# Optimization experiments

Measured on AMD Instinct MI355X. Metric: run time of the kernel, lower is better.

The kernel has to match this reference:

```python
import jax, jax.numpy as jnp
import numpy as np

B, N, F = 2, 100000, 64
E = 800000
E_OUT, N_OUT = 16, 64


def setup_inputs() -> dict:
    key = jax.random.key(0)
    ks = jax.random.split(key, 8)
    x = jax.random.normal(ks[0], (B, N, F), dtype=jnp.float32)
    edge_src = jax.random.randint(ks[1], (E,), 0, N, dtype=jnp.int32)
    edge_target = jax.random.randint(ks[2], (E,), 0, N, dtype=jnp.int32)
    edge_weight = jax.random.uniform(ks[3], (E, 1), dtype=jnp.float32)
    in_dim = 2 * F + 1  # 129
    W_e = jax.random.normal(ks[4], (in_dim, E_OUT), dtype=jnp.float32) / np.sqrt(in_dim)
    b_e = jnp.zeros((E_OUT,), dtype=jnp.float32)
    W_n = jax.random.normal(ks[5], (E_OUT, N_OUT), dtype=jnp.float32) / np.sqrt(E_OUT)
    b_n = jnp.zeros((N_OUT,), dtype=jnp.float32)
    return {"x": x, "edge_src": edge_src, "edge_target": edge_target,
            "edge_weight": edge_weight, "W_e": W_e, "b_e": b_e,
            "W_n": W_n, "b_n": b_n}


def reference(x, edge_src, edge_target, edge_weight, W_e, b_e, W_n, b_n):
    # gather endpoint features: [B, E, F]
    node_src = x[:, edge_src]
    node_target = x[:, edge_target]
    # per-edge learned scalar weight broadcast over batch: [B, E, 1]
    ew = jnp.broadcast_to(edge_weight[None, :, :], (x.shape[0], edge_weight.shape[0], 1))
    h = jnp.concatenate([node_src, node_target, ew], axis=-1)  # [B, E, 2F+1]
    h = jax.nn.sigmoid(h @ W_e + b_e)                           # edge MLP -> [B, E, 16]
    # scatter_add(+h at target) + scatter_add(-h at src) -> [B, N, 16]
    agg = jnp.zeros((x.shape[0], x.shape[1], h.shape[-1]), dtype=h.dtype)
    agg = agg.at[:, edge_target].add(h).at[:, edge_src].add(-h)
    out = jax.nn.sigmoid(agg @ W_n + b_n)                       # node MLP -> [B, N, out_dim]
    return out
```

## Files before the change

### kernel.cpp

```cpp
#include <hip/hip_runtime.h>
#include <hip/hip_fp16.h>

#define NB 2
#define NN 100000
#define NF 64
#define NE 800000
#define EO 16
#define NO 64
#define QS 512.0f

__device__ __forceinline__ float sigmoidf(float v) {
    return 1.0f / (1.0f + __expf(-v));
}

__global__ __launch_bounds__(256) void pre_kernel(
    const float* __restrict__ x, const float* __restrict__ We,
    const float* __restrict__ be, __half* __restrict__ P1h,
    __half* __restrict__ P2h, float4* __restrict__ aggz)
{
    int u = blockIdx.x * 256 + threadIdx.x;
    if (u >= NB * NN) return;
    int b = u >= NN;
    int n = u - b * NN;

    if (!b) {
        float4 z = make_float4(0.f, 0.f, 0.f, 0.f);
#pragma unroll
        for (int q = 0; q < 4; ++q) aggz[(size_t)n * 4 + q] = z;
    }

    float a1[EO], a2[EO];
#pragma unroll
    for (int k = 0; k < EO; ++k) { a1[k] = 0.f; a2[k] = be[k]; }

    const float* row = x + (size_t)u * NF;
#pragma unroll 4
    for (int j4 = 0; j4 < 16; ++j4) {
        float4 v = *(const float4*)(row + 4 * j4);
        const float* w1 = We + (size_t)(4 * j4) * EO;
        const float* w2 = We + (size_t)(NF + 4 * j4) * EO;
#pragma unroll
        for (int jj = 0; jj < 4; ++jj) {
            float vv = ((const float*)&v)[jj];
#pragma unroll
            for (int k = 0; k < EO; ++k) {
                a1[k] += vv * w1[jj * EO + k];
                a2[k] += vv * w2[jj * EO + k];
            }
        }
    }

    __half2 h1[8], h2[8];
#pragma unroll
    for (int i = 0; i < 8; ++i) {
        h1[i] = __floats2half2_rn(a1[2 * i], a1[2 * i + 1]);
        h2[i] = __floats2half2_rn(a2[2 * i], a2[2 * i + 1]);
    }
    __half* p1 = P1h + (size_t)n * (NB * EO) + b * EO;
    __half* p2 = P2h + (size_t)n * (NB * EO) + b * EO;
    *(float4*)(p1)     = ((float4*)h1)[0];
    *(float4*)(p1 + 8) = ((float4*)h1)[1];
    *(float4*)(p2)     = ((float4*)h2)[0];
    *(float4*)(p2 + 8) = ((float4*)h2)[1];
}

__global__ __launch_bounds__(256) void edge_kernel(
    const int* __restrict__ esrc, const int* __restrict__ etgt,
    const float* __restrict__ ew, const __half* __restrict__ P1h,
    const __half* __restrict__ P2h, const float* __restrict__ We,
    unsigned long long* __restrict__ agg)
{
    __shared__ unsigned long long hbuf[256 * 9];
    __shared__ int snode[256];
    __shared__ int tnode[256];

    int tid = threadIdx.x;
    int e = blockIdx.x * 256 + tid;
    int s = esrc[e];
    int t = etgt[e];
    float w = ew[e];
    snode[tid] = s;
    tnode[tid] = t;

    const float* wr = We + (size_t)2 * NF * EO;

    float4 sv[4], tv[4];
    const float4* p1 = (const float4*)(P1h + (size_t)s * (NB * EO));
    const float4* p2 = (const float4*)(P2h + (size_t)t * (NB * EO));
#pragma unroll
    for (int i = 0; i < 4; ++i) { sv[i] = p1[i]; tv[i] = p2[i]; }

    const __half2* sh = (const __half2*)sv;
    const __half2* th = (const __half2*)tv;
    float hs[NB * EO];
#pragma unroll
    for (int i = 0; i < 16; ++i) {
        float2 fs = __half22float2(sh[i]);
        float2 ft = __half22float2(th[i]);
        hs[2 * i]     = sigmoidf(fs.x + ft.x + w * wr[(2 * i) & 15]);
        hs[2 * i + 1] = sigmoidf(fs.y + ft.y + w * wr[(2 * i + 1) & 15]);
    }

#pragma unroll
    for (int j = 0; j < 8; ++j) {
        long long q0 = __float2int_rn(hs[4 * j + 0] * QS);
        long long q1 = __float2int_rn(hs[4 * j + 1] * QS);
        long long q2 = __float2int_rn(hs[4 * j + 2] * QS);
        long long q3 = __float2int_rn(hs[4 * j + 3] * QS);
        hbuf[tid * 9 + j] =
            (unsigned long long)(q0 + (q1 << 16) + (q2 << 32) + (q3 << 48));
    }
    __syncthreads();

    int g = tid >> 3;
    int k8 = tid & 7;
#pragma unroll
    for (int i = 0; i < 8; ++i) {
        int el = g + (i << 5);
        unsigned long long v = hbuf[el * 9 + k8];
        int tt = tnode[el];
        int ss = snode[el];
        atomicAdd(agg + (size_t)tt * 8 + k8, v);
        atomicAdd(agg + (size_t)ss * 8 + k8, 0ULL - v);
    }
}

__global__ __launch_bounds__(256) void node_kernel(
    const unsigned long long* __restrict__ agg, const float* __restrict__ Wn,
    const float* __restrict__ bn, float* __restrict__ out)
{
    __shared__ float wn[EO * NO];
    int tid = threadIdx.x;
    {
        float4 wv = ((const float4*)Wn)[tid];
        wv.x *= (1.0f / QS); wv.y *= (1.0f / QS);
        wv.z *= (1.0f / QS); wv.w *= (1.0f / QS);
        *(float4*)(wn + tid * 4) = wv;
    }
    __syncthreads();

    int u = blockIdx.x * 256 + tid;
    int row = u >> 4;
    int q = u & 15;
    int b = row >= NN;
    int n = row - b * NN;

    const unsigned long long* ar = agg + ((size_t)n * NB + b) * 4;
    ulonglong2 w01 = ((const ulonglong2*)ar)[0];
    ulonglong2 w23 = ((const ulonglong2*)ar)[1];
    unsigned long long ww[4] = { w01.x, w01.y, w23.x, w23.y };

    float a[EO];
#pragma unroll
    for (int j = 0; j < 4; ++j) {
        unsigned long long wv = ww[j];
        int s0 = (short)(unsigned short)wv;
        wv = (wv - (unsigned long long)(long long)s0) >> 16;
        int s1 = (short)(unsigned short)wv;
        wv = (wv - (unsigned long long)(long long)s1) >> 16;
        int s2 = (short)(unsigned short)wv;
        wv = (wv - (unsigned long long)(long long)s2) >> 16;
        int s3 = (short)(unsigned short)wv;
        a[4 * j + 0] = (float)s0;
        a[4 * j + 1] = (float)s1;
        a[4 * j + 2] = (float)s2;
        a[4 * j + 3] = (float)s3;
    }

    float4 acc = *(const float4*)(bn + q * 4);
#pragma unroll
    for (int k = 0; k < EO; ++k) {
        float ak = a[k];
        float4 wv = *(const float4*)(wn + k * NO + q * 4);
        acc.x += ak * wv.x;
        acc.y += ak * wv.y;
        acc.z += ak * wv.z;
        acc.w += ak * wv.w;
    }
    float4 o = make_float4(sigmoidf(acc.x), sigmoidf(acc.y),
                           sigmoidf(acc.z), sigmoidf(acc.w));
    *(float4*)(out + (size_t)row * NO + q * 4) = o;
}

extern "C" void kernel_launch(void* const* d_in, const int* in_sizes, int n_in,
                              void* d_out, int out_size, void* d_ws, size_t ws_size,
                              hipStream_t stream) {
    const float* x    = (const float*)d_in[0];
    const int*   esrc = (const int*)d_in[1];
    const int*   etgt = (const int*)d_in[2];
    const float* ew   = (const float*)d_in[3];
    const float* We   = (const float*)d_in[4];
    const float* be   = (const float*)d_in[5];
    const float* Wn   = (const float*)d_in[6];
    const float* bn   = (const float*)d_in[7];
    float* out = (float*)d_out;

    unsigned long long* agg = (unsigned long long*)d_ws;
    __half* P1h = (__half*)((char*)d_ws + (size_t)NN * 8 * sizeof(unsigned long long));
    __half* P2h = P1h + (size_t)NN * NB * EO;

    pre_kernel<<<(NB * NN + 255) / 256, 256, 0, stream>>>(x, We, be, P1h, P2h,
                                                          (float4*)agg);
    edge_kernel<<<NE / 256, 256, 0, stream>>>(esrc, etgt, ew, P1h, P2h, We, agg);
    node_kernel<<<NB * NN * 16 / 256, 256, 0, stream>>>(agg, Wn, bn, out);
}
```

Measured before the change: 223.1 us.

## Stage node rows in shared memory for pre-kernel and split edge kernel into chunks

The pre-kernel now loads 64 node rows per block into padded shared memory. Each wave computes 8 of the 32 projection outputs (one half of W_e and one k-half), so per-thread register pressure drops and the global x reads are coalesced. Zeroing the aggregation buffer is spread over all threads. The edge kernel is launched as 8 sequential chunks via a block offset, perhaps to improve atomic locality or L2 residency, at the cost of extra launch overhead.

```diff
diff --git a/kernel.cpp b/kernel.cpp
--- a/kernel.cpp
+++ b/kernel.cpp
@@ -16,55 +16,58 @@
 __global__ __launch_bounds__(256) void pre_kernel(
     const float* __restrict__ x, const float* __restrict__ We,
     const float* __restrict__ be, __half* __restrict__ P1h,
-    __half* __restrict__ P2h, float4* __restrict__ aggz)
+    __half* __restrict__ P2h, unsigned long long* __restrict__ aggz)
 {
-    int u = blockIdx.x * 256 + threadIdx.x;
-    if (u >= NB * NN) return;
-    int b = u >= NN;
-    int n = u - b * NN;
-
-    if (!b) {
-        float4 z = make_float4(0.f, 0.f, 0.f, 0.f);
-#pragma unroll
-        for (int q = 0; q < 4; ++q) aggz[(size_t)n * 4 + q] = z;
-    }
-
-    float a1[EO], a2[EO];
-#pragma unroll
-    for (int k = 0; k < EO; ++k) { a1[k] = 0.f; a2[k] = be[k]; }
-
-    const float* row = x + (size_t)u * NF;
-#pragma unroll 4
+    __shared__ float xs[64 * 68];
+    int tid = threadIdx.x;
+    int bid = blockIdx.x;
+
+    aggz[(size_t)bid * 256 + tid] = 0ULL;
+
+    const float4* xsrc = (const float4*)(x + (size_t)bid * 64 * NF);
+#pragma unroll
+    for (int i = 0; i < 4; ++i) {
+        int f = i * 256 + tid;
+        int r = f >> 4, c4 = f & 15;
+        float4 v = xsrc[f];
+        *(float4*)&xs[r * 68 + c4 * 4] = v;
+    }
+    __syncthreads();
+
+    int r = tid & 63;
+    int wv = __builtin_amdgcn_readfirstlane(tid >> 6);
+    int half = wv & 1;
+    int kh = wv >> 1;
+    const float* wb = We + (size_t)half * NF * EO + kh * 8;
+
+    float a[8];
+#pragma unroll
+    for (int k = 0; k < 8; ++k) a[k] = half ? be[kh * 8 + k] : 0.f;
+
+#pragma unroll 2
     for (int j4 = 0; j4 < 16; ++j4) {
-        float4 v = *(const float4*)(row + 4 * j4);
-        const float* w1 = We + (size_t)(4 * j4) * EO;
-        const float* w2 = We + (size_t)(NF + 4 * j4) * EO;
+        float4 v = *(const float4*)&xs[r * 68 + j4 * 4];
 #pragma unroll
         for (int jj = 0; jj < 4; ++jj) {
             float vv = ((const float*)&v)[jj];
 #pragma unroll
-            for (int k = 0; k < EO; ++k) {
-                a1[k] += vv * w1[jj * EO + k];
-                a2[k] += vv * w2[jj * EO + k];
-            }
+            for (int k = 0; k < 8; ++k)
+                a[k] += vv * wb[(4 * j4 + jj) * EO + k];
         }
     }
 
-    __half2 h1[8], h2[8];
-#pragma unroll
-    for (int i = 0; i < 8; ++i) {
-        h1[i] = __floats2half2_rn(a1[2 * i], a1[2 * i + 1]);
-        h2[i] = __floats2half2_rn(a2[2 * i], a2[2 * i + 1]);
-    }
-    __half* p1 = P1h + (size_t)n * (NB * EO) + b * EO;
-    __half* p2 = P2h + (size_t)n * (NB * EO) + b * EO;
-    *(float4*)(p1)     = ((float4*)h1)[0];
-    *(float4*)(p1 + 8) = ((float4*)h1)[1];
-    *(float4*)(p2)     = ((float4*)h2)[0];
-    *(float4*)(p2 + 8) = ((float4*)h2)[1];
+    int rg = bid * 64 + r;
+    int b = rg >= NN;
+    int n = rg - b * NN;
+    __half2 o[4];
+#pragma unroll
+    for (int i = 0; i < 4; ++i) o[i] = __floats2half2_rn(a[2 * i], a[2 * i + 1]);
+    __half* dst = (half ? P2h : P1h) + (size_t)n * (NB * EO) + b * EO + kh * 8;
+    *(float4*)dst = *(float4*)o;
 }
 
 __global__ __launch_bounds__(256) void edge_kernel(
+    int blockBase,
     const int* __restrict__ esrc, const int* __restrict__ etgt,
     const float* __restrict__ ew, const __half* __restrict__ P1h,
     const __half* __restrict__ P2h, const float* __restrict__ We,
@@ -75,7 +78,7 @@
     __shared__ int tnode[256];
 
     int tid = threadIdx.x;
-    int e = blockIdx.x * 256 + tid;
+    int e = (blockBase + blockIdx.x) * 256 + tid;
     int s = esrc[e];
     int t = etgt[e];
     float w = ew[e];
@@ -199,8 +202,13 @@
     __half* P1h = (__half*)((char*)d_ws + (size_t)NN * 8 * sizeof(unsigned long long));
     __half* P2h = P1h + (size_t)NN * NB * EO;
 
-    pre_kernel<<<(NB * NN + 255) / 256, 256, 0, stream>>>(x, We, be, P1h, P2h,
-                                                          (float4*)agg);
-    edge_kernel<<<NE / 256, 256, 0, stream>>>(esrc, etgt, ew, P1h, P2h, We, agg);
+    pre_kernel<<<NB * NN / 64, 256, 0, stream>>>(x, We, be, P1h, P2h, agg);
+
+    static const int bases[9] = {0, 391, 782, 1173, 1564, 1955, 2345, 2735, 3125};
+    for (int c = 0; c < 8; ++c) {
+        edge_kernel<<<bases[c + 1] - bases[c], 256, 0, stream>>>(
+            bases[c], esrc, etgt, ew, P1h, P2h, We, agg);
+    }
+
     node_kernel<<<NB * NN * 16 / 256, 256, 0, stream>>>(agg, Wn, bn, out);
 }
```

New measurement: 248.1 us. 1.11x slower.
